# Kernel tuning notes

Hardware: AMD Instinct MI355X
Metric: run time of the kernel (lower is better)

The kernel has to match this reference:

```python
import jax, jax.numpy as jnp
import numpy as np

D_MODEL = 1024
NUM_HEADS = 16
DEPTH = D_MODEL // NUM_HEADS


def setup_inputs() -> dict:
    key = jax.random.key(0)
    ks = jax.random.split(key, 6)
    B, S = 2, 2048
    scale = 1.0 / np.sqrt(D_MODEL)
    return {
        "q": jax.random.normal(ks[0], (B, S, D_MODEL), jnp.float32),
        "k": jax.random.normal(ks[1], (B, S, D_MODEL), jnp.float32),
        "v": jax.random.normal(ks[2], (B, S, D_MODEL), jnp.float32),
        "wq": jax.random.normal(ks[3], (D_MODEL, D_MODEL), jnp.float32) * scale,
        "wk": jax.random.normal(ks[4], (D_MODEL, D_MODEL), jnp.float32) * scale,
        "wv": jax.random.normal(ks[5], (D_MODEL, D_MODEL), jnp.float32) * scale,
    }


def reference(q, k, v, wq, wk, wv):
    B, S, _ = q.shape
    # Linear projections (nn.Linear: x @ W.T), then split heads -> [B,H,S,depth]
    def split(x):
        return x.reshape(B, -1, NUM_HEADS, DEPTH).transpose(0, 2, 1, 3)
    Q = split(q @ wq.T)
    K = split(k @ wk.T)
    V = split(v @ wv.T)
    scores = jnp.einsum("bhqd,bhkd->bhqk", Q, K) / np.sqrt(DEPTH).astype(np.float32)
    attn = jax.nn.softmax(scores, axis=-1)
    out = jnp.einsum("bhqk,bhkd->bhqd", attn, V)
    # merge heads; note: original forward never applies self.dense
    return out.transpose(0, 2, 1, 3).reshape(B, S, D_MODEL)
```

## Files before the change

### kernel.cpp

```cpp
#include <hip/hip_runtime.h>
#include <hip/hip_bf16.h>
#include <stdint.h>

#define B_SZ 2
#define S_LEN 2048
#define DM 1024
#define NH 16
#define DEPTH 64
#define M_ROWS (B_SZ * S_LEN)
#define SCALE_Q 0.1803368801111144f

typedef __attribute__((ext_vector_type(8))) short bf16x8;
typedef __attribute__((ext_vector_type(4))) float f32x4;
typedef __attribute__((ext_vector_type(16))) float f32x16;

__device__ __forceinline__ unsigned short f2bf(float x) {
    union { float f; unsigned u; } a; a.f = x;
    unsigned r = a.u + 0x7FFF + ((a.u >> 16) & 1);
    return (unsigned short)(r >> 16);
}

__device__ __forceinline__ bf16x8 u4_to_bf8(uint4 u) {
    union { uint4 a; bf16x8 b; } c; c.a = u; return c.b;
}

__device__ __forceinline__ unsigned cvtpk_bf16(float lo, float hi) {
    unsigned r;
    asm("v_cvt_pk_bf16_f32 %0, %1, %2" : "=v"(r) : "v"(lo), "v"(hi));
    return r;
}

__device__ __forceinline__ void permswap32(unsigned &a, unsigned &b) {
    auto r = __builtin_amdgcn_permlane32_swap(a, b, false, false);
    a = r[0]; b = r[1];
}

__device__ __forceinline__ void async_ld16(const unsigned short* g, void* l) {
    __builtin_amdgcn_global_load_lds(
        (const __attribute__((address_space(1))) void*)g,
        (__attribute__((address_space(3))) void*)l,
        16, 0, 0);
}


__global__ __launch_bounds__(256)
void convert_kernel(const float* __restrict__ q, const float* __restrict__ k,
                    const float* __restrict__ v, const float* __restrict__ wq,
                    const float* __restrict__ wk, const float* __restrict__ wv,
                    unsigned short* __restrict__ dst) {
    const int z = blockIdx.y;
    const float* src = (z == 0) ? q : (z == 1) ? k : (z == 2) ? v
                     : (z == 3) ? wq : (z == 4) ? wk : wv;
    const size_t n4  = (z < 3) ? ((size_t)M_ROWS * DM / 4) : ((size_t)DM * DM / 4);
    const size_t off = (z < 3) ? ((size_t)z * M_ROWS * DM)
                               : ((size_t)3 * M_ROWS * DM + (size_t)(z - 3) * DM * DM);
    unsigned short* d = dst + off;
    const size_t stride = (size_t)gridDim.x * blockDim.x;
    for (size_t i = (size_t)blockIdx.x * blockDim.x + threadIdx.x; i < n4; i += stride) {
        float4 x = ((const float4*)src)[i];
        ushort4 p;
        p.x = f2bf(x.x); p.y = f2bf(x.y); p.z = f2bf(x.z); p.w = f2bf(x.w);
        ((ushort4*)d)[i] = p;
    }
}

__global__ __launch_bounds__(256)
void proj_gemm3_kernel(const unsigned short* __restrict__ Xall,
                       const unsigned short* __restrict__ Wall,
                       unsigned short* __restrict__ Call,
                       unsigned short* __restrict__ Vtp) {
    __shared__ unsigned short SMEM[2 * 128 * 64];
    unsigned short* As = SMEM;
    unsigned short* Bs = SMEM + 128 * 64;

    const int lin = blockIdx.x + (blockIdx.y << 5) + blockIdx.z * 256;
    const int v96 = (lin & 7) * 96 + (lin >> 3);
    const int xb  = v96 & 31;
    const int yb  = (v96 >> 5) & 7;
    const int z   = v96 >> 8;

    const unsigned short* X = Xall + (size_t)z * M_ROWS * DM;
    const unsigned short* W = Wall + (size_t)z * DM * DM;
    unsigned short* C = Call + (size_t)z * M_ROWS * DM;

    const int tid  = threadIdx.x;
    const int wave = tid >> 6;
    const int lane = tid & 63;
    const int l32  = lane & 31;
    const int s    = lane >> 5;
    const int m0 = xb * 128;
    const int n0 = yb * 128;
    const int wm = (wave >> 1) * 64;
    const int wn = (wave & 1) * 64;

    const int r8 = lane >> 3;
    const int sc = (lane & 7) ^ r8;

    f32x16 acc[2][2];
#pragma unroll
    for (int mi = 0; mi < 2; ++mi)
#pragma unroll
        for (int ni = 0; ni < 2; ++ni)
#pragma unroll
            for (int r = 0; r < 16; ++r) acc[mi][ni][r] = 0.f;

    for (int k0 = 0; k0 < DM; k0 += 64) {
#pragma unroll
        for (int i = 0; i < 4; ++i) {
            const int r = i * 32 + wave * 8 + r8;
            async_ld16(X + (size_t)(m0 + r) * DM + k0 + sc * 8,
                       (char*)As + i * 4096 + wave * 1024);
            async_ld16(W + (size_t)(n0 + r) * DM + k0 + sc * 8,
                       (char*)Bs + i * 4096 + wave * 1024);
        }
        __syncthreads();

#pragma unroll
        for (int ch = 0; ch < 4; ++ch) {
            bf16x8 af[2], bfr[2];
#pragma unroll
            for (int mi = 0; mi < 2; ++mi) {
                const int row = wm + mi * 32 + l32;
                af[mi] = *(const bf16x8*)&As[row * 64 + (((2 * ch + s) ^ (row & 7)) * 8)];
            }
#pragma unroll
            for (int ni = 0; ni < 2; ++ni) {
                const int row = wn + ni * 32 + l32;
                bfr[ni] = *(const bf16x8*)&Bs[row * 64 + (((2 * ch + s) ^ (row & 7)) * 8)];
            }
#pragma unroll
            for (int mi = 0; mi < 2; ++mi)
#pragma unroll
                for (int ni = 0; ni < 2; ++ni)
                    acc[mi][ni] = __builtin_amdgcn_mfma_f32_32x32x16_bf16(
                        af[mi], bfr[ni], acc[mi][ni], 0, 0, 0);
        }
        __syncthreads();
    }

    if (z < 2) {
        const float scale = (z == 0) ? SCALE_Q : 1.0f;
#pragma unroll
        for (int mi = 0; mi < 2; ++mi)
#pragma unroll
            for (int ni = 0; ni < 2; ++ni)
#pragma unroll
                for (int r = 0; r < 16; ++r) {
                    const int row = m0 + wm + mi * 32 + (r & 3) + 8 * (r >> 2) + 4 * s;
                    const int col = n0 + wn + ni * 32 + l32;
                    C[(size_t)row * DM + col] = f2bf(acc[mi][ni][r] * scale);
                }
    } else {
        const int b2  = m0 >> 11;
        const int h2  = (n0 + wn) >> 6;
        const int t0l = (m0 & 2047) + wm;
        unsigned short* Tr = SMEM + wave * 2368;
        const int d_sub = lane >> 3;
        const int tc    = lane & 7;
        unsigned short* VtH =
            Vtp + (size_t)((b2 * NH + h2) * DEPTH) * S_LEN;
#pragma unroll
        for (int ni = 0; ni < 2; ++ni) {
#pragma unroll
            for (int mi = 0; mi < 2; ++mi)
#pragma unroll
                for (int r = 0; r < 16; ++r) {
                    const int tl = mi * 32 + (r & 3) + 8 * (r >> 2) + 4 * s;
                    Tr[tl * 37 + l32] = f2bf(acc[mi][ni][r]);
                }
            asm volatile("s_waitcnt lgkmcnt(0)" ::: "memory");
            __builtin_amdgcn_sched_barrier(0);
#pragma unroll
            for (int di = 0; di < 4; ++di) {
                const int dl = d_sub + di * 8;
                unsigned short tmp[8];
#pragma unroll
                for (int j = 0; j < 8; ++j)
                    tmp[j] = Tr[(tc * 8 + j) * 37 + dl];
                *(bf16x8*)&VtH[(size_t)(ni * 32 + dl) * S_LEN + t0l + tc * 8] =
                    *(const bf16x8*)tmp;
            }
            asm volatile("s_waitcnt lgkmcnt(0)" ::: "memory");
            __builtin_amdgcn_sched_barrier(0);
        }
    }
}

__global__ __launch_bounds__(256, 4)
void attn8_kernel(const unsigned short* __restrict__ Qp,
                  const unsigned short* __restrict__ Kp,
                  const unsigned short* __restrict__ Vt,
                  float* __restrict__ out,
                  float* __restrict__ Op1,
                  float* __restrict__ lp) {
    __shared__ __align__(16) char smem[32768];
    unsigned short* Ks = (unsigned short*)smem;
    unsigned short* Vs = (unsigned short*)(smem + 16384);

    const int tid  = threadIdx.x;
    const int w    = tid >> 6;
    const int lane = tid & 63;
    const int l32  = lane & 31;
    const int s    = lane >> 5;
    const int r8   = lane >> 3;
    const int sc   = (lane & 7) ^ r8;

    const int lin = blockIdx.x + (blockIdx.y << 4) + (blockIdx.z << 8);
    const int v   = ((lin & 7) << 7) + (lin >> 3);
    const int qt  = v & 15;
    const int h   = (v >> 4) & 15;
    const int z   = v >> 8;

    const int q0 = qt * 128 + w * 32;
    const int b     = z >> 1;
    const int split = z & 1;
    const int tbase = split * 1024;

    const unsigned short* Kg = Kp + (size_t)(b * S_LEN + tbase) * DM + h * DEPTH;
    const unsigned short* Vg = Vt + (size_t)((b * NH + h) * DEPTH) * S_LEN + tbase;
    float* obase = split ? Op1 : out;
    float* lbase = lp + (size_t)split * M_ROWS * NH;

    bf16x8 qf[4];
    {
        const unsigned short* p =
            Qp + (size_t)(b * S_LEN + q0 + l32) * DM + h * DEPTH;
#pragma unroll
        for (int ch = 0; ch < 4; ++ch)
            qf[ch] = *(const bf16x8*)(p + ch * 16 + s * 8);
    }

    f32x16 oacc[2];
    float lacc = 0.f;
#pragma unroll
    for (int db = 0; db < 2; ++db)
#pragma unroll
        for (int r = 0; r < 16; ++r) oacc[db][r] = 0.f;

#pragma unroll
    for (int i = 0; i < 2; ++i) {
        async_ld16(Kg + (size_t)(w * 16 + i * 8 + r8) * DM + sc * 8,
                   (char*)smem + w * 2048 + i * 1024);
        async_ld16(Vg + (size_t)(w * 16 + i * 8 + r8) * S_LEN + sc * 8,
                   (char*)smem + 16384 + w * 2048 + i * 1024);
    }

    for (int it = 0; it < 16; ++it) {
        const int cb = it & 1;

        asm volatile("s_waitcnt vmcnt(0) lgkmcnt(0)" ::: "memory");
        __syncthreads();

        if (it < 15) {
            const int tn = (it + 1) * 64;
            char* kd = (char*)smem + (cb ^ 1) * 8192 + w * 2048;
            char* vd = (char*)smem + 16384 + (cb ^ 1) * 8192 + w * 2048;
#pragma unroll
            for (int i = 0; i < 2; ++i) {
                async_ld16(Kg + (size_t)(tn + w * 16 + i * 8 + r8) * DM + sc * 8,
                           kd + i * 1024);
                async_ld16(Vg + (size_t)(w * 16 + i * 8 + r8) * S_LEN + tn + sc * 8,
                           vd + i * 1024);
            }
        }

        const unsigned short* Kb = Ks + cb * 4096;
        const unsigned short* Vb = Vs + cb * 4096;

        f32x16 sv0, sv1;
#pragma unroll
        for (int r = 0; r < 16; ++r) { sv0[r] = 0.f; sv1[r] = 0.f; }
        __builtin_amdgcn_s_setprio(1);
#pragma unroll
        for (int ch = 0; ch < 4; ++ch) {
            bf16x8 kf0 = *(const bf16x8*)
                &Kb[l32 * 64 + (((2 * ch + s) ^ (l32 & 7)) * 8)];
            bf16x8 kf1 = *(const bf16x8*)
                &Kb[2048 + l32 * 64 + (((2 * ch + s) ^ (l32 & 7)) * 8)];
            sv0 = __builtin_amdgcn_mfma_f32_32x32x16_bf16(kf0, qf[ch], sv0, 0, 0, 0);
            sv1 = __builtin_amdgcn_mfma_f32_32x32x16_bf16(kf1, qf[ch], sv1, 0, 0, 0);
        }
        __builtin_amdgcn_s_setprio(0);

        unsigned pw[2][8];
#pragma unroll
        for (int th = 0; th < 2; ++th) {
            float p[16];
#pragma unroll
            for (int r = 0; r < 16; ++r)
                p[r] = __builtin_amdgcn_exp2f(th ? sv1[r] : sv0[r]);
            lacc += ((p[0] + p[1]) + (p[2] + p[3]))
                  + ((p[4] + p[5]) + (p[6] + p[7]))
                  + ((p[8] + p[9]) + (p[10] + p[11]))
                  + ((p[12] + p[13]) + (p[14] + p[15]));
            unsigned a0 = cvtpk_bf16(p[0],  p[1]);
            unsigned b0 = cvtpk_bf16(p[4],  p[5]);
            unsigned a1 = cvtpk_bf16(p[2],  p[3]);
            unsigned b1 = cvtpk_bf16(p[6],  p[7]);
            unsigned a2 = cvtpk_bf16(p[8],  p[9]);
            unsigned b2 = cvtpk_bf16(p[12], p[13]);
            unsigned a3 = cvtpk_bf16(p[10], p[11]);
            unsigned b3 = cvtpk_bf16(p[14], p[15]);
            permswap32(a0, b0);
            permswap32(a1, b1);
            permswap32(a2, b2);
            permswap32(a3, b3);
            pw[th][0] = a0; pw[th][1] = a1; pw[th][2] = b0; pw[th][3] = b1;
            pw[th][4] = a2; pw[th][5] = a3; pw[th][6] = b2; pw[th][7] = b3;
        }

#pragma unroll
        for (int th = 0; th < 2; ++th) {
            const int vcb = th * 4;
#pragma unroll
            for (int ch = 0; ch < 2; ++ch) {
                uint4 pu;
                pu.x = pw[th][ch * 4 + 0];
                pu.y = pw[th][ch * 4 + 1];
                pu.z = pw[th][ch * 4 + 2];
                pu.w = pw[th][ch * 4 + 3];
                bf16x8 pf = u4_to_bf8(pu);
                __builtin_amdgcn_s_setprio(1);
#pragma unroll
                for (int db = 0; db < 2; ++db) {
                    const int drow = db * 32 + l32;
                    bf16x8 vf = *(const bf16x8*)
                        &Vb[drow * 64 + (((vcb + 2 * ch + s) ^ (l32 & 7)) * 8)];
                    oacc[db] = __builtin_amdgcn_mfma_f32_32x32x16_bf16(
                        vf, pf, oacc[db], 0, 0, 0);
                }
                __builtin_amdgcn_s_setprio(0);
            }
        }
    }

    asm volatile("s_waitcnt vmcnt(0)" ::: "memory");

    const float l0 = lacc + __shfl_xor(lacc, 32, 64);
    if (s == 0)
        lbase[(size_t)(b * S_LEN + q0 + l32) * NH + h] = l0;

    __syncthreads();
    float* Of = (float*)(smem + w * 4608);
#pragma unroll
    for (int c = 0; c < 2; ++c) {
        if ((l32 >> 4) == c) {
            const int qh = l32 & 15;
#pragma unroll
            for (int db = 0; db < 2; ++db)
#pragma unroll
                for (int m = 0; m < 4; ++m) {
                    float4 v4;
                    v4.x = oacc[db][4 * m + 0];
                    v4.y = oacc[db][4 * m + 1];
                    v4.z = oacc[db][4 * m + 2];
                    v4.w = oacc[db][4 * m + 3];
                    *(float4*)&Of[qh * 68 + db * 32 + 8 * m + 4 * s] = v4;
                }
        }
        asm volatile("" ::: "memory");
#pragma unroll
        for (int i = 0; i < 4; ++i) {
            const int row = i * 4 + (lane >> 4);
            const int c4 = lane & 15;
            float4 v4 = *(const float4*)&Of[row * 68 + c4 * 4];
            *(float4*)&obase[(size_t)(b * S_LEN + q0 + c * 16 + row) * DM
                             + h * DEPTH + c4 * 4] = v4;
        }
        asm volatile("" ::: "memory");
    }
}

__global__ __launch_bounds__(256)
void combine_kernel(float* __restrict__ out, const float* __restrict__ Op1,
                    const float* __restrict__ lp) {
    const int i4 = blockIdx.x * 256 + threadIdx.x;
    const int row = i4 >> 8;
    const int c4  = i4 & 255;
    const int h   = c4 >> 4;
    const float l = lp[row * NH + h] + lp[M_ROWS * NH + row * NH + h];
    const float inv = 1.0f / l;
    float4 a = ((const float4*)out)[i4];
    float4 bq = ((const float4*)Op1)[i4];
    a.x = (a.x + bq.x) * inv;
    a.y = (a.y + bq.y) * inv;
    a.z = (a.z + bq.z) * inv;
    a.w = (a.w + bq.w) * inv;
    ((float4*)out)[i4] = a;
}

#define LDK 72

__global__ __launch_bounds__(256)
void proj_gemm_kernel(const float* __restrict__ q, const float* __restrict__ k,
                      const float* __restrict__ v, const float* __restrict__ wq,
                      const float* __restrict__ wk, const float* __restrict__ wv,
                      unsigned short* __restrict__ Qp, unsigned short* __restrict__ Kp,
                      unsigned short* __restrict__ Vp) {
    __shared__ unsigned short As[128 * LDK];
    __shared__ unsigned short Bs[128 * LDK];

    const int z = blockIdx.z;
    const float* __restrict__ X = (z == 0) ? q : (z == 1) ? k : v;
    const float* __restrict__ W = (z == 0) ? wq : (z == 1) ? wk : wv;
    unsigned short* __restrict__ C = (z == 0) ? Qp : (z == 1) ? Kp : Vp;

    const int tid  = threadIdx.x;
    const int wave = tid >> 6;
    const int lane = tid & 63;
    const int quad = lane >> 4;
    const int l16  = lane & 15;
    const int m0 = blockIdx.x * 128;
    const int n0 = blockIdx.y * 128;
    const int wm = (wave >> 1) * 64;
    const int wn = (wave & 1) * 64;

    f32x4 acc[4][4];
#pragma unroll
    for (int mt = 0; mt < 4; ++mt)
#pragma unroll
        for (int nt = 0; nt < 4; ++nt)
            acc[mt][nt] = (f32x4){0.f, 0.f, 0.f, 0.f};

    for (int k0 = 0; k0 < DM; k0 += 64) {
#pragma unroll
        for (int vv = 0; vv < 8; ++vv) {
            int vecid = tid + 256 * vv;
            int r  = vecid >> 4;
            int c4 = vecid & 15;
            const float4 xa = *(const float4*)&X[(size_t)(m0 + r) * DM + k0 + c4 * 4];
            ushort4 pa;
            pa.x = f2bf(xa.x); pa.y = f2bf(xa.y); pa.z = f2bf(xa.z); pa.w = f2bf(xa.w);
            *(ushort4*)&As[r * LDK + c4 * 4] = pa;
            const float4 xb = *(const float4*)&W[(size_t)(n0 + r) * DM + k0 + c4 * 4];
            ushort4 pb;
            pb.x = f2bf(xb.x); pb.y = f2bf(xb.y); pb.z = f2bf(xb.z); pb.w = f2bf(xb.w);
            *(ushort4*)&Bs[r * LDK + c4 * 4] = pb;
        }
        __syncthreads();

#pragma unroll
        for (int kc = 0; kc < 2; ++kc) {
            bf16x8 af[4], bfr[4];
#pragma unroll
            for (int mt = 0; mt < 4; ++mt)
                af[mt] = *(const bf16x8*)&As[(wm + mt * 16 + l16) * LDK + kc * 32 + quad * 8];
#pragma unroll
            for (int nt = 0; nt < 4; ++nt)
                bfr[nt] = *(const bf16x8*)&Bs[(wn + nt * 16 + l16) * LDK + kc * 32 + quad * 8];
#pragma unroll
            for (int mt = 0; mt < 4; ++mt)
#pragma unroll
                for (int nt = 0; nt < 4; ++nt)
                    acc[mt][nt] = __builtin_amdgcn_mfma_f32_16x16x32_bf16(
                        af[mt], bfr[nt], acc[mt][nt], 0, 0, 0);
        }
        __syncthreads();
    }

#pragma unroll
    for (int mt = 0; mt < 4; ++mt)
#pragma unroll
        for (int nt = 0; nt < 4; ++nt)
#pragma unroll
            for (int r = 0; r < 4; ++r) {
                int row = m0 + wm + mt * 16 + quad * 4 + r;
                int col = n0 + wn + nt * 16 + l16;
                C[(size_t)row * DM + col] = f2bf(acc[mt][nt][r]);
            }
}

__global__ __launch_bounds__(256)
void attn_kernel(const unsigned short* __restrict__ Qp,
                 const unsigned short* __restrict__ Kp,
                 const unsigned short* __restrict__ Vp,
                 float* __restrict__ out) {
    __shared__ unsigned short Ks[64 * LDK];
    __shared__ unsigned short Vtl[64 * LDK];
    __shared__ unsigned short Ps[4 * 16 * LDK];

    const int tid  = threadIdx.x;
    const int wave = tid >> 6;
    const int lane = tid & 63;
    const int quad = lane >> 4;
    const int l16  = lane & 15;
    const int q0 = blockIdx.x * 64;
    const int h  = blockIdx.y;
    const int b  = blockIdx.z;
    const int wbase = wave * 16 * LDK;

    bf16x8 qf[2];
    {
        size_t row = (size_t)b * S_LEN + q0 + wave * 16 + l16;
        const unsigned short* p = Qp + row * DM + h * DEPTH;
        qf[0] = *(const bf16x8*)(p + quad * 8);
        qf[1] = *(const bf16x8*)(p + 32 + quad * 8);
    }

    float m_i[4], l_i[4];
    f32x4 accO[4];
#pragma unroll
    for (int r = 0; r < 4; ++r) { m_i[r] = -1e30f; l_i[r] = 0.f; }
#pragma unroll
    for (int f = 0; f < 4; ++f) accO[f] = (f32x4){0.f, 0.f, 0.f, 0.f};

    for (int t0 = 0; t0 < S_LEN; t0 += 64) {
#pragma unroll
        for (int vv = 0; vv < 2; ++vv) {
            int vecid = tid + 256 * vv;
            int r  = vecid >> 3;
            int cv = vecid & 7;
            size_t grow = (size_t)(b * S_LEN + t0 + r) * DM + h * DEPTH + cv * 8;
            *(bf16x8*)&Ks[r * LDK + cv * 8] = *(const bf16x8*)(Kp + grow);
            bf16x8 vvv = *(const bf16x8*)(Vp + grow);
#pragma unroll
            for (int j = 0; j < 8; ++j)
                Vtl[(cv * 8 + j) * LDK + r] = ((const unsigned short*)&vvv)[j];
        }
        __syncthreads();

        f32x4 sc4[4];
#pragma unroll
        for (int nt = 0; nt < 4; ++nt) {
            f32x4 a = (f32x4){0.f, 0.f, 0.f, 0.f};
            bf16x8 kf0 = *(const bf16x8*)&Ks[(nt * 16 + l16) * LDK + quad * 8];
            bf16x8 kf1 = *(const bf16x8*)&Ks[(nt * 16 + l16) * LDK + 32 + quad * 8];
            a = __builtin_amdgcn_mfma_f32_16x16x32_bf16(qf[0], kf0, a, 0, 0, 0);
            a = __builtin_amdgcn_mfma_f32_16x16x32_bf16(qf[1], kf1, a, 0, 0, 0);
            sc4[nt] = a;
        }
#pragma unroll
        for (int nt = 0; nt < 4; ++nt)
#pragma unroll
            for (int r = 0; r < 4; ++r) sc4[nt][r] *= 0.125f;

#pragma unroll
        for (int r = 0; r < 4; ++r) {
            float mx = fmaxf(fmaxf(sc4[0][r], sc4[1][r]), fmaxf(sc4[2][r], sc4[3][r]));
#pragma unroll
            for (int off = 1; off < 16; off <<= 1)
                mx = fmaxf(mx, __shfl_xor(mx, off, 64));
            float mnew = fmaxf(m_i[r], mx);
            float alpha = __expf(m_i[r] - mnew);
            float rs = 0.f;
#pragma unroll
            for (int nt = 0; nt < 4; ++nt) {
                float p = __expf(sc4[nt][r] - mnew);
                sc4[nt][r] = p;
                rs += p;
            }
#pragma unroll
            for (int off = 1; off < 16; off <<= 1)
                rs += __shfl_xor(rs, off, 64);
            l_i[r] = l_i[r] * alpha + rs;
            m_i[r] = mnew;
#pragma unroll
            for (int f = 0; f < 4; ++f) accO[f][r] *= alpha;
        }

#pragma unroll
        for (int nt = 0; nt < 4; ++nt)
#pragma unroll
            for (int r = 0; r < 4; ++r)
                Ps[wbase + (quad * 4 + r) * LDK + nt * 16 + l16] = f2bf(sc4[nt][r]);
        __syncthreads();

        bf16x8 pf0 = *(const bf16x8*)&Ps[wbase + l16 * LDK + quad * 8];
        bf16x8 pf1 = *(const bf16x8*)&Ps[wbase + l16 * LDK + 32 + quad * 8];
#pragma unroll
        for (int f = 0; f < 4; ++f) {
            bf16x8 vf0 = *(const bf16x8*)&Vtl[(f * 16 + l16) * LDK + quad * 8];
            bf16x8 vf1 = *(const bf16x8*)&Vtl[(f * 16 + l16) * LDK + 32 + quad * 8];
            accO[f] = __builtin_amdgcn_mfma_f32_16x16x32_bf16(pf0, vf0, accO[f], 0, 0, 0);
            accO[f] = __builtin_amdgcn_mfma_f32_16x16x32_bf16(pf1, vf1, accO[f], 0, 0, 0);
        }
        __syncthreads();
    }

#pragma unroll
    for (int f = 0; f < 4; ++f)
#pragma unroll
        for (int r = 0; r < 4; ++r) {
            size_t row = (size_t)b * S_LEN + q0 + wave * 16 + quad * 4 + r;
            out[row * DM + h * DEPTH + f * 16 + l16] = accO[f][r] / l_i[r];
        }
}

extern "C" void kernel_launch(void* const* d_in, const int* in_sizes, int n_in,
                              void* d_out, int out_size, void* d_ws, size_t ws_size,
                              hipStream_t stream) {
    const float* q  = (const float*)d_in[0];
    const float* k  = (const float*)d_in[1];
    const float* v  = (const float*)d_in[2];
    const float* wq = (const float*)d_in[3];
    const float* wk = (const float*)d_in[4];
    const float* wv = (const float*)d_in[5];
    float* out = (float*)d_out;

    unsigned short* ws = (unsigned short*)d_ws;
    const size_t NPROJ = (size_t)M_ROWS * DM;
    const size_t NW    = (size_t)DM * DM;

    const size_t need = (3 * NPROJ + 3 * NW + 3 * NPROJ) * sizeof(unsigned short);

    if (ws_size >= need) {
        unsigned short* Xbf = ws;
        unsigned short* Wbf = ws + 3 * NPROJ;
        unsigned short* Cp  = ws + 3 * NPROJ + 3 * NW;
        unsigned short* Qp  = Cp;
        unsigned short* Kp  = Cp + NPROJ;
        unsigned short* Vt  = Cp + 2 * NPROJ;
        float*          Op1 = (float*)(ws + NPROJ);
        float*          lp  = (float*)(ws + 3 * NPROJ);

        convert_kernel<<<dim3(256, 6), 256, 0, stream>>>(q, k, v, wq, wk, wv, Xbf);
        proj_gemm3_kernel<<<dim3(M_ROWS / 128, DM / 128, 3), 256, 0, stream>>>(
            Xbf, Wbf, Cp, Vt);
        attn8_kernel<<<dim3(S_LEN / 128, NH, 4), 256, 0, stream>>>(
            Qp, Kp, Vt, out, Op1, lp);
        combine_kernel<<<dim3(M_ROWS * DM / 4 / 256), 256, 0, stream>>>(out, Op1, lp);
    } else {
        unsigned short* Qp = ws;
        unsigned short* Kp = ws + NPROJ;
        unsigned short* Vp = ws + 2 * NPROJ;
        proj_gemm_kernel<<<dim3(M_ROWS / 128, DM / 128, 3), 256, 0, stream>>>(
            q, k, v, wq, wk, wv, Qp, Kp, Vp);
        attn_kernel<<<dim3(S_LEN / 64, NH, B_SZ), 256, 0, stream>>>(Qp, Kp, Vp, out);
    }
}
```

Measured before the change: 200.3 us.

## Double-buffer LDS tiles in projection GEMM and drop block swizzle

The projection GEMM now uses two LDS buffers, so the global-to-LDS async loads for the next K tile are issued while MFMAs run on the current one. This hides load latency and needs only one barrier per iteration instead of two. It also removes the XCD-aware block-index remapping in favour of plain blockIdx mapping, which may change L2 locality. LDS use doubles to 64KB per block, which can lower occupancy, and the V-transpose scratch offsets are moved to fit the new layout.

```diff
diff --git a/kernel.cpp b/kernel.cpp
--- a/kernel.cpp
+++ b/kernel.cpp
@@ -69,16 +69,9 @@
                        const unsigned short* __restrict__ Wall,
                        unsigned short* __restrict__ Call,
                        unsigned short* __restrict__ Vtp) {
-    __shared__ unsigned short SMEM[2 * 128 * 64];
-    unsigned short* As = SMEM;
-    unsigned short* Bs = SMEM + 128 * 64;
-
-    const int lin = blockIdx.x + (blockIdx.y << 5) + blockIdx.z * 256;
-    const int v96 = (lin & 7) * 96 + (lin >> 3);
-    const int xb  = v96 & 31;
-    const int yb  = (v96 >> 5) & 7;
-    const int z   = v96 >> 8;
-
+    __shared__ unsigned short SMEM[4 * 128 * 64];
+
+    const int z = blockIdx.z;
     const unsigned short* X = Xall + (size_t)z * M_ROWS * DM;
     const unsigned short* W = Wall + (size_t)z * DM * DM;
     unsigned short* C = Call + (size_t)z * M_ROWS * DM;
@@ -88,8 +81,8 @@
     const int lane = tid & 63;
     const int l32  = lane & 31;
     const int s    = lane >> 5;
-    const int m0 = xb * 128;
-    const int n0 = yb * 128;
+    const int m0 = blockIdx.x * 128;
+    const int n0 = blockIdx.y * 128;
     const int wm = (wave >> 1) * 64;
     const int wn = (wave & 1) * 64;
 
@@ -104,16 +97,37 @@
 #pragma unroll
             for (int r = 0; r < 16; ++r) acc[mi][ni][r] = 0.f;
 
-    for (int k0 = 0; k0 < DM; k0 += 64) {
-#pragma unroll
-        for (int i = 0; i < 4; ++i) {
-            const int r = i * 32 + wave * 8 + r8;
-            async_ld16(X + (size_t)(m0 + r) * DM + k0 + sc * 8,
-                       (char*)As + i * 4096 + wave * 1024);
-            async_ld16(W + (size_t)(n0 + r) * DM + k0 + sc * 8,
-                       (char*)Bs + i * 4096 + wave * 1024);
-        }
+#pragma unroll
+    for (int i = 0; i < 4; ++i) {
+        const int r = i * 32 + wave * 8 + r8;
+        async_ld16(X + (size_t)(m0 + r) * DM + sc * 8,
+                   (char*)SMEM + i * 4096 + wave * 1024);
+        async_ld16(W + (size_t)(n0 + r) * DM + sc * 8,
+                   (char*)SMEM + 32768 + i * 4096 + wave * 1024);
+    }
+
+    for (int kk = 0; kk < 16; ++kk) {
+        const int cb = kk & 1;
+
+        asm volatile("s_waitcnt vmcnt(0) lgkmcnt(0)" ::: "memory");
         __syncthreads();
+
+        if (kk < 15) {
+            const int k0 = (kk + 1) * 64;
+            char* ad = (char*)SMEM + (cb ^ 1) * 16384;
+            char* bd = (char*)SMEM + 32768 + (cb ^ 1) * 16384;
+#pragma unroll
+            for (int i = 0; i < 4; ++i) {
+                const int r = i * 32 + wave * 8 + r8;
+                async_ld16(X + (size_t)(m0 + r) * DM + k0 + sc * 8,
+                           ad + i * 4096 + wave * 1024);
+                async_ld16(W + (size_t)(n0 + r) * DM + k0 + sc * 8,
+                           bd + i * 4096 + wave * 1024);
+            }
+        }
+
+        const unsigned short* As = SMEM + cb * 8192;
+        const unsigned short* Bs = SMEM + 16384 + cb * 8192;
 
 #pragma unroll
         for (int ch = 0; ch < 4; ++ch) {
@@ -135,7 +149,6 @@
                     acc[mi][ni] = __builtin_amdgcn_mfma_f32_32x32x16_bf16(
                         af[mi], bfr[ni], acc[mi][ni], 0, 0, 0);
         }
-        __syncthreads();
     }
 
     if (z < 2) {
@@ -154,7 +167,7 @@
         const int b2  = m0 >> 11;
         const int h2  = (n0 + wn) >> 6;
         const int t0l = (m0 & 2047) + wm;
-        unsigned short* Tr = SMEM + wave * 2368;
+        unsigned short* Tr = SMEM + (wave >> 1) * 16384 + (wave & 1) * 2368;
         const int d_sub = lane >> 3;
         const int tc    = lane & 7;
         unsigned short* VtH =
```

New measurement: 186.5 us. 6.9% less time.
